# Optimization experiments

Hardware: AMD Instinct MI355X
Metric: run time of the kernel (lower is better)

## Reference

```python
import jax, jax.numpy as jnp
import numpy as np

B, L, H, HEADS, BLOCKS, TSPAN = 8, 256, 256, 4, 2, 512
D = H // HEADS
BIG_NEG = jnp.float32(-2.0**32 + 1)


def _layernorm(x, g, b, eps=1e-8):
    m = x.mean(-1, keepdims=True)
    v = ((x - m) ** 2).mean(-1, keepdims=True)
    return (x - m) / jnp.sqrt(v + eps) * g + b


def _forward(seq_emb, Wq, bq, Wk, bk, Wv, bv, ln1_g, ln1_b, ln2_g, ln2_b,
             W1, b1, W2, b2, pos_K, pos_V, tK_emb, tV_emb, lnf_g, lnf_b,
             mask, time_matrices):
    # relative time-interval embeddings: [B,L,L,H] -> per-head [B,L,L,heads,D]
    tmKh = tK_emb[time_matrices].reshape(B, L, L, HEADS, D)
    tmVh = tV_emb[time_matrices].reshape(B, L, L, HEADS, D)
    posKh = pos_K.reshape(L, HEADS, D)  # abs position embs (positions = arange(L))
    posVh = pos_V.reshape(L, HEADS, D)
    keep = (~mask)[..., None].astype(seq_emb.dtype)  # [B,L,1], True mask = pad
    causal = ~jnp.tril(jnp.ones((L, L), dtype=bool))  # True above diagonal
    x = seq_emb * keep
    scale = jnp.sqrt(jnp.float32(D))
    for i in range(BLOCKS):
        q = _layernorm(x, ln1_g[i], ln1_b[i])  # queries normalized, keys/values raw
        Qh = (q @ Wq[i].T + bq[i]).reshape(B, L, HEADS, D)
        Kh = (x @ Wk[i].T + bk[i]).reshape(B, L, HEADS, D)
        Vh = (x @ Wv[i].T + bv[i]).reshape(B, L, HEADS, D)
        aw = (jnp.einsum('bqhd,bkhd->bhqk', Qh, Kh)
              + jnp.einsum('bqhd,khd->bhqk', Qh, posKh)
              + jnp.einsum('bqhd,bqkhd->bhqk', Qh, tmKh)) / scale
        aw = jnp.where(mask[:, None, :, None] | causal[None, None], BIG_NEG, aw)
        p = jax.nn.softmax(aw, axis=-1)
        out = (jnp.einsum('bhqk,bkhd->bqhd', p, Vh)
               + jnp.einsum('bhqk,khd->bqhd', p, posVh)
               + jnp.einsum('bhqk,bqkhd->bqhd', p, tmVh)).reshape(B, L, H)
        x = q + out
        x = _layernorm(x, ln2_g[i], ln2_b[i])
        h = jax.nn.relu(jnp.einsum('bld,od->blo', x, W1[i]) + b1[i])  # Conv1d k=1 == Linear
        x = jnp.einsum('bld,od->blo', h, W2[i]) + b2[i] + x
        x = x * keep
    return _layernorm(x, lnf_g, lnf_b)


def setup_inputs():
    key = jax.random.key(0)
    ks = jax.random.split(key, 24)
    s = 0.02
    nrm = lambda k, shape: jax.random.normal(k, shape, dtype=jnp.float32) * s
    inp = {}
    inp['mask'] = jax.random.uniform(ks[0], (B, L)) < 0.1
    inp['seq_emb'] = jax.random.normal(ks[1], (B, L, H), dtype=jnp.float32)
    inp['log_seqs'] = jax.random.randint(ks[2], (B, L), 0, 1000)
    inp['time_matrices'] = jax.random.randint(ks[3], (B, L, L), 0, TSPAN + 1).astype(jnp.int32)
    inp['time_attn'] = 0
    inp['Wq'] = nrm(ks[4], (BLOCKS, H, H)); inp['bq'] = jnp.zeros((BLOCKS, H), jnp.float32)
    inp['Wk'] = nrm(ks[5], (BLOCKS, H, H)); inp['bk'] = jnp.zeros((BLOCKS, H), jnp.float32)
    inp['Wv'] = nrm(ks[6], (BLOCKS, H, H)); inp['bv'] = jnp.zeros((BLOCKS, H), jnp.float32)
    inp['ln1_g'] = jnp.ones((BLOCKS, H), jnp.float32); inp['ln1_b'] = jnp.zeros((BLOCKS, H), jnp.float32)
    inp['ln2_g'] = jnp.ones((BLOCKS, H), jnp.float32); inp['ln2_b'] = jnp.zeros((BLOCKS, H), jnp.float32)
    inp['W1'] = nrm(ks[7], (BLOCKS, H, H)); inp['b1'] = jnp.zeros((BLOCKS, H), jnp.float32)
    inp['W2'] = nrm(ks[8], (BLOCKS, H, H)); inp['b2'] = jnp.zeros((BLOCKS, H), jnp.float32)
    inp['pos_K'] = nrm(ks[9], (L, H)); inp['pos_V'] = nrm(ks[10], (L, H))
    inp['tK_emb'] = nrm(ks[11], (TSPAN + 1, H)); inp['tV_emb'] = nrm(ks[12], (TSPAN + 1, H))
    inp['lnf_g'] = jnp.ones((H,), jnp.float32); inp['lnf_b'] = jnp.zeros((H,), jnp.float32)
    return inp


def reference(mask, seq_emb, log_seqs, time_matrices, time_attn,
              Wq, bq, Wk, bk, Wv, bv, ln1_g, ln1_b, ln2_g, ln2_b,
              W1, b1, W2, b2, pos_K, pos_V, tK_emb, tV_emb, lnf_g, lnf_b):
    return _forward(seq_emb, Wq, bq, Wk, bk, Wv, bv, ln1_g, ln1_b, ln2_g, ln2_b,
                    W1, b1, W2, b2, pos_K, pos_V, tK_emb, tV_emb, lnf_g, lnf_b,
                    mask, time_matrices)
```

## Files before the change

### kernel.cpp

```cpp
#include <hip/hip_runtime.h>

#define BIG_NEG_F (-4294967296.0f)

typedef __attribute__((ext_vector_type(8))) short bf16x8;
typedef __attribute__((ext_vector_type(4))) float f32x4;

__device__ __forceinline__ float wave_sum(float v) {
#pragma unroll
    for (int m = 32; m; m >>= 1) v += __shfl_xor(v, m, 64);
    return v;
}
__device__ __forceinline__ float wave_max(float v) {
#pragma unroll
    for (int m = 32; m; m >>= 1) v = fmaxf(v, __shfl_xor(v, m, 64));
    return v;
}

__device__ __forceinline__ unsigned int pack2(float a, float b) {
    return (__float_as_uint(b) & 0xffff0000u) | (__float_as_uint(a) >> 16);
}
__device__ __forceinline__ float hipart(float x) {
    return __uint_as_float(__float_as_uint(x) & 0xffff0000u);
}
__device__ __forceinline__ void store_pair(unsigned short* hp, unsigned short* lp,
                                           float4 a, float4 b) {
    uint4 h;
    h.x = pack2(a.x, a.y); h.y = pack2(a.z, a.w);
    h.z = pack2(b.x, b.y); h.w = pack2(b.z, b.w);
    float lax = a.x - hipart(a.x), lay = a.y - hipart(a.y);
    float laz = a.z - hipart(a.z), law = a.w - hipart(a.w);
    float lbx = b.x - hipart(b.x), lby = b.y - hipart(b.y);
    float lbz = b.z - hipart(b.z), lbw = b.w - hipart(b.w);
    uint4 l;
    l.x = pack2(lax, lay); l.y = pack2(laz, law);
    l.z = pack2(lbx, lby); l.w = pack2(lbz, lbw);
    *(uint4*)hp = h;
    *(uint4*)lp = l;
}

__global__ __launch_bounds__(256) void prep_ln_kernel(const float* __restrict__ seq,
                                                      const unsigned char* __restrict__ mraw,
                                                      unsigned char* __restrict__ mout,
                                                      float* __restrict__ X, float* __restrict__ Q,
                                                      const float* __restrict__ g,
                                                      const float* __restrict__ be) {
    __shared__ int flags[2];
    __shared__ float ws[8];
    int row = blockIdx.x, tid = threadIdx.x;
    if (tid == 0) { flags[0] = 0; flags[1] = 0; }
    __syncthreads();
    for (int i = tid; i < 2048; i += 256) {
        if (mraw[i]) {
            if (i & 3) atomicOr(&flags[0], 1);
            else if (i & 4) atomicOr(&flags[1], 1);
        }
    }
    __syncthreads();
    int mode = flags[0] ? 0 : (flags[1] ? 1 : 2);
    unsigned char mrow = (mode == 0) ? mraw[row] : (mode == 1) ? mraw[row * 4] : mraw[row * 8];
    if (tid == 0) mout[row] = mrow ? 1 : 0;
    int idx = row * 256 + tid;
    int w = tid >> 6, lane = tid & 63;
    float v = mrow ? 0.f : seq[idx];
    X[idx] = v;
    float s = wave_sum(v);
    if (lane == 0) ws[w] = s;
    __syncthreads();
    float mean = (ws[0] + ws[1] + ws[2] + ws[3]) * (1.f / 256.f);
    float d = v - mean;
    float s2 = wave_sum(d * d);
    if (lane == 0) ws[4 + w] = s2;
    __syncthreads();
    float var = (ws[4] + ws[5] + ws[6] + ws[7]) * (1.f / 256.f);
    Q[idx] = d / sqrtf(var + 1e-8f) * g[tid] + be[tid];
}

__global__ __launch_bounds__(256) void ln_kernel(const float* __restrict__ X, float* __restrict__ Y,
                                                 const float* __restrict__ g,
                                                 const float* __restrict__ be) {
    __shared__ float ws[8];
    int row = blockIdx.x, tid = threadIdx.x;
    int idx = row * 256 + tid;
    int w = tid >> 6, lane = tid & 63;
    float v = X[idx];
    float s = wave_sum(v);
    if (lane == 0) ws[w] = s;
    __syncthreads();
    float mean = (ws[0] + ws[1] + ws[2] + ws[3]) * (1.f / 256.f);
    float d = v - mean;
    float s2 = wave_sum(d * d);
    if (lane == 0) ws[4 + w] = s2;
    __syncthreads();
    float var = (ws[4] + ws[5] + ws[6] + ws[7]) * (1.f / 256.f);
    Y[idx] = d / sqrtf(var + 1e-8f) * g[tid] + be[tid];
}

struct GemmJob {
    const float* A;
    const float* W;
    const float* bias;
    const float* pos;
    const float* res;
    const unsigned char* maskm;
    float* C;
    int relu;
};

__global__ __launch_bounds__(256) void gemm_mfma_kernel(GemmJob j0, GemmJob j1, GemmJob j2) {
    GemmJob J = (blockIdx.z == 0) ? j0 : (blockIdx.z == 1 ? j1 : j2);
    __shared__ unsigned short Ah[64][72], Al[64][72], Wh[64][72], Wl[64][72];
    int tid = threadIdx.x;
    int n0 = blockIdx.x * 64, m0 = blockIdx.y * 64;
    int w = tid >> 6, lane = tid & 63;
    int wm = w >> 1, wn = w & 1;
    int srow = tid >> 2, sq = tid & 3;
    const float* Asrc = J.A + (m0 + srow) * 256 + sq * 16;
    const float* Wsrc = J.W + (n0 + srow) * 256 + sq * 16;
    float4 ar0 = *(const float4*)(Asrc),      ar1 = *(const float4*)(Asrc + 4),
           ar2 = *(const float4*)(Asrc + 8),  ar3 = *(const float4*)(Asrc + 12);
    float4 wr0 = *(const float4*)(Wsrc),      wr1 = *(const float4*)(Wsrc + 4),
           wr2 = *(const float4*)(Wsrc + 8),  wr3 = *(const float4*)(Wsrc + 12);
    f32x4 acc[2][2] = {};
    int r15 = lane & 15, hgrp = (lane >> 4) << 3;
    for (int kt = 0; kt < 4; ++kt) {
        if (kt) __syncthreads();
        store_pair(&Ah[srow][sq * 16],     &Al[srow][sq * 16],     ar0, ar1);
        store_pair(&Ah[srow][sq * 16 + 8], &Al[srow][sq * 16 + 8], ar2, ar3);
        store_pair(&Wh[srow][sq * 16],     &Wl[srow][sq * 16],     wr0, wr1);
        store_pair(&Wh[srow][sq * 16 + 8], &Wl[srow][sq * 16 + 8], wr2, wr3);
        __syncthreads();
        if (kt < 3) {
            int ko = (kt + 1) * 64;
            ar0 = *(const float4*)(Asrc + ko);      ar1 = *(const float4*)(Asrc + ko + 4);
            ar2 = *(const float4*)(Asrc + ko + 8);  ar3 = *(const float4*)(Asrc + ko + 12);
            wr0 = *(const float4*)(Wsrc + ko);      wr1 = *(const float4*)(Wsrc + ko + 4);
            wr2 = *(const float4*)(Wsrc + ko + 8);  wr3 = *(const float4*)(Wsrc + ko + 12);
        }
#pragma unroll
        for (int s = 0; s < 2; ++s) {
            int ko = s * 32 + hgrp;
            bf16x8 ah0 = *(const bf16x8*)&Ah[wm * 32 + r15][ko];
            bf16x8 ah1 = *(const bf16x8*)&Ah[wm * 32 + 16 + r15][ko];
            bf16x8 al0 = *(const bf16x8*)&Al[wm * 32 + r15][ko];
            bf16x8 al1 = *(const bf16x8*)&Al[wm * 32 + 16 + r15][ko];
            bf16x8 bh0 = *(const bf16x8*)&Wh[wn * 32 + r15][ko];
            bf16x8 bh1 = *(const bf16x8*)&Wh[wn * 32 + 16 + r15][ko];
            bf16x8 bl0 = *(const bf16x8*)&Wl[wn * 32 + r15][ko];
            bf16x8 bl1 = *(const bf16x8*)&Wl[wn * 32 + 16 + r15][ko];
            acc[0][0] = __builtin_amdgcn_mfma_f32_16x16x32_bf16(ah0, bh0, acc[0][0], 0, 0, 0);
            acc[0][0] = __builtin_amdgcn_mfma_f32_16x16x32_bf16(ah0, bl0, acc[0][0], 0, 0, 0);
            acc[0][0] = __builtin_amdgcn_mfma_f32_16x16x32_bf16(al0, bh0, acc[0][0], 0, 0, 0);
            acc[0][1] = __builtin_amdgcn_mfma_f32_16x16x32_bf16(ah0, bh1, acc[0][1], 0, 0, 0);
            acc[0][1] = __builtin_amdgcn_mfma_f32_16x16x32_bf16(ah0, bl1, acc[0][1], 0, 0, 0);
            acc[0][1] = __builtin_amdgcn_mfma_f32_16x16x32_bf16(al0, bh1, acc[0][1], 0, 0, 0);
            acc[1][0] = __builtin_amdgcn_mfma_f32_16x16x32_bf16(ah1, bh0, acc[1][0], 0, 0, 0);
            acc[1][0] = __builtin_amdgcn_mfma_f32_16x16x32_bf16(ah1, bl0, acc[1][0], 0, 0, 0);
            acc[1][0] = __builtin_amdgcn_mfma_f32_16x16x32_bf16(al1, bh0, acc[1][0], 0, 0, 0);
            acc[1][1] = __builtin_amdgcn_mfma_f32_16x16x32_bf16(ah1, bh1, acc[1][1], 0, 0, 0);
            acc[1][1] = __builtin_amdgcn_mfma_f32_16x16x32_bf16(ah1, bl1, acc[1][1], 0, 0, 0);
            acc[1][1] = __builtin_amdgcn_mfma_f32_16x16x32_bf16(al1, bh1, acc[1][1], 0, 0, 0);
        }
    }
#pragma unroll
    for (int mf = 0; mf < 2; ++mf) {
#pragma unroll
        for (int nf = 0; nf < 2; ++nf) {
            int col = n0 + wn * 32 + nf * 16 + r15;
            int rowb = m0 + wm * 32 + mf * 16 + ((lane >> 4) << 2);
            float bcol = J.bias[col];
            f32x4 a = acc[mf][nf];
#pragma unroll
            for (int rr = 0; rr < 4; ++rr) {
                int m = rowb + rr;
                float v = a[rr] + bcol;
                if (J.pos) v += J.pos[(m & 255) * 256 + col];
                if (J.relu) v = fmaxf(v, 0.f);
                if (J.res) v += J.res[m * 256 + col];
                if (J.maskm && J.maskm[m]) v = 0.f;
                J.C[m * 256 + col] = v;
            }
        }
    }
}

__global__ __launch_bounds__(256, 8) void attn_kernel(
    const float* __restrict__ Q, const float* __restrict__ Kp, const float* __restrict__ Vp,
    const float* __restrict__ qres, const int* __restrict__ tm,
    const float* __restrict__ tK, const float* __restrict__ tV,
    const float* __restrict__ g2, const float* __restrict__ b2,
    float* __restrict__ X2) {
    int bid = (int)blockIdx.x;
    int b = bid & 7;
    int i6 = bid >> 3;
    int jj6 = i6 & 31, a6 = i6 >> 5;
    int q0m = jj6 * 4 + (a6 >> 1);
    int qpos = (a6 & 1) ? q0m : 255 - q0m;
    int tid = threadIdx.x, w = tid >> 6, lane = tid & 63;
    __shared__ float qrow[256];
    __shared__ int   stm[256];
    __shared__ float p[4][264];
    __shared__ float opart[4][256];
    __shared__ float denom[4];
    __shared__ float lnws[8];

    int rowbase = (b * 256 + qpos) * 256;
    qrow[tid] = Q[rowbase + tid];
    {
        int t = tm[rowbase + tid];
        stm[tid] = t < 0 ? 0 : (t > 512 ? 512 : t);
    }
    __syncthreads();

    {
        int h = lane >> 4;
        const float* qr = qrow + lane * 4;
        float q0 = qr[0], q1 = qr[1], q2 = qr[2], q3 = qr[3];
        const float* Kb  = Kp + (size_t)(b << 8) * 256 + lane * 4;
        const float* tKb = tK + lane * 4;
        int nact = (qpos >= w) ? ((qpos - w) >> 2) + 1 : 0;
        int i = 0;
        for (; i + 2 <= nact; i += 2) {
            int k0 = w + 4 * i;
            float4 kv0 = *(const float4*)(Kb + (k0    ) * 256);
            float4 kv1 = *(const float4*)(Kb + (k0 + 4) * 256);
            float4 t0 = *(const float4*)(tKb + stm[k0    ] * 256);
            float4 t1 = *(const float4*)(tKb + stm[k0 + 4] * 256);
            float s0 = q0 * (kv0.x + t0.x) + q1 * (kv0.y + t0.y) + q2 * (kv0.z + t0.z) + q3 * (kv0.w + t0.w);
            float s1 = q0 * (kv1.x + t1.x) + q1 * (kv1.y + t1.y) + q2 * (kv1.z + t1.z) + q3 * (kv1.w + t1.w);
            s0 += __shfl_xor(s0, 1, 64); s1 += __shfl_xor(s1, 1, 64);
            s0 += __shfl_xor(s0, 2, 64); s1 += __shfl_xor(s1, 2, 64);
            s0 += __shfl_xor(s0, 4, 64); s1 += __shfl_xor(s1, 4, 64);
            s0 += __shfl_xor(s0, 8, 64); s1 += __shfl_xor(s1, 8, 64);
            if ((lane & 15) == 0) {
                p[h][k0    ] = s0 * 0.125f;
                p[h][k0 + 4] = s1 * 0.125f;
            }
        }
        if (i < nact) {
            int k = w + 4 * i;
            float4 kv = *(const float4*)(Kb + k * 256);
            float4 t4 = *(const float4*)(tKb + stm[k] * 256);
            float s = q0 * (kv.x + t4.x) + q1 * (kv.y + t4.y) + q2 * (kv.z + t4.z) + q3 * (kv.w + t4.w);
            s += __shfl_xor(s, 1, 64);
            s += __shfl_xor(s, 2, 64);
            s += __shfl_xor(s, 4, 64);
            s += __shfl_xor(s, 8, 64);
            if ((lane & 15) == 0) p[h][k] = s * 0.125f;
        }
    }
    __syncthreads();

    {
        float* ph = &p[w][0];
        float v0 = (lane       <= qpos) ? ph[lane      ] : BIG_NEG_F;
        float v1 = (lane + 64  <= qpos) ? ph[lane + 64 ] : BIG_NEG_F;
        float v2 = (lane + 128 <= qpos) ? ph[lane + 128] : BIG_NEG_F;
        float v3 = (lane + 192 <= qpos) ? ph[lane + 192] : BIG_NEG_F;
        float mx = wave_max(fmaxf(fmaxf(v0, v1), fmaxf(v2, v3)));
        float e0 = __expf(v0 - mx), e1 = __expf(v1 - mx), e2 = __expf(v2 - mx), e3 = __expf(v3 - mx);
        ph[lane] = e0; ph[lane + 64] = e1; ph[lane + 128] = e2; ph[lane + 192] = e3;
        float ssum = wave_sum(e0 + e1 + e2 + e3);
        if (lane == 0) denom[w] = ssum;
    }
    __syncthreads();

    {
        int hh = lane >> 4;
        const float* Vb  = Vp + (size_t)(b << 8) * 256 + lane * 4;
        const float* tVb = tV + lane * 4;
        const float* prow = &p[hh][0];
        float4 a0 = {0.f, 0.f, 0.f, 0.f}, a1 = a0;
        int cnt = (qpos >= w) ? ((qpos - w) >> 2) + 1 : 0;
        int i = 0;
        for (; i + 2 <= cnt; i += 2) {
            int k0 = w + 4 * i;
            float p0 = prow[k0], p1 = prow[k0 + 4];
            float4 v0 = *(const float4*)(Vb + (k0    ) * 256);
            float4 v1 = *(const float4*)(Vb + (k0 + 4) * 256);
            float4 u0 = *(const float4*)(tVb + stm[k0    ] * 256);
            float4 u1 = *(const float4*)(tVb + stm[k0 + 4] * 256);
            a0.x += p0 * (v0.x + u0.x); a0.y += p0 * (v0.y + u0.y); a0.z += p0 * (v0.z + u0.z); a0.w += p0 * (v0.w + u0.w);
            a1.x += p1 * (v1.x + u1.x); a1.y += p1 * (v1.y + u1.y); a1.z += p1 * (v1.z + u1.z); a1.w += p1 * (v1.w + u1.w);
        }
        if (i < cnt) {
            int k2 = w + 4 * i;
            float pk = prow[k2];
            float4 v = *(const float4*)(Vb + k2 * 256);
            float4 t = *(const float4*)(tVb + stm[k2] * 256);
            a0.x += pk * (v.x + t.x);
            a0.y += pk * (v.y + t.y);
            a0.z += pk * (v.z + t.z);
            a0.w += pk * (v.w + t.w);
        }
        float4 o;
        o.x = a0.x + a1.x;
        o.y = a0.y + a1.y;
        o.z = a0.z + a1.z;
        o.w = a0.w + a1.w;
        *(float4*)&opart[w][lane * 4] = o;
    }
    __syncthreads();

    {
        int d = tid, h = tid >> 6;
        float tot = opart[0][d] + opart[1][d] + opart[2][d] + opart[3][d];
        float xv = qres[rowbase + d] + tot / denom[h];
        float s = wave_sum(xv);
        if (lane == 0) lnws[w] = s;
        __syncthreads();
        float mean = (lnws[0] + lnws[1] + lnws[2] + lnws[3]) * (1.f / 256.f);
        float dd = xv - mean;
        float s2 = wave_sum(dd * dd);
        if (lane == 0) lnws[4 + w] = s2;
        __syncthreads();
        float var = (lnws[4] + lnws[5] + lnws[6] + lnws[7]) * (1.f / 256.f);
        X2[rowbase + d] = dd / sqrtf(var + 1e-8f) * g2[d] + b2[d];
    }
}

extern "C" void kernel_launch(void* const* d_in, const int* in_sizes, int n_in,
                              void* d_out, int out_size, void* d_ws, size_t ws_size,
                              hipStream_t stream) {
    const unsigned char* mask_raw = (const unsigned char*)d_in[0];
    const float* seq  = (const float*)d_in[1];
    const int*   tm   = (const int*)d_in[3];
    const float* Wq   = (const float*)d_in[5];
    const float* bq   = (const float*)d_in[6];
    const float* Wk   = (const float*)d_in[7];
    const float* bk   = (const float*)d_in[8];
    const float* Wv   = (const float*)d_in[9];
    const float* bv   = (const float*)d_in[10];
    const float* ln1g = (const float*)d_in[11];
    const float* ln1b = (const float*)d_in[12];
    const float* ln2g = (const float*)d_in[13];
    const float* ln2b = (const float*)d_in[14];
    const float* W1   = (const float*)d_in[15];
    const float* b1   = (const float*)d_in[16];
    const float* W2   = (const float*)d_in[17];
    const float* b2   = (const float*)d_in[18];
    const float* posK = (const float*)d_in[19];
    const float* posV = (const float*)d_in[20];
    const float* tK   = (const float*)d_in[21];
    const float* tV   = (const float*)d_in[22];
    const float* lnfg = (const float*)d_in[23];
    const float* lnfb = (const float*)d_in[24];

    const int NEL = 8 * 256 * 256;
    float* x   = (float*)d_ws;
    float* q   = x   + NEL;
    float* Qb  = q   + NEL;
    float* KpB = Qb  + NEL;
    float* VpB = KpB + NEL;
    float* x2  = VpB + NEL;
    float* hb  = x2  + NEL;
    unsigned char* mask = (unsigned char*)(hb + NEL);

    dim3 gQKV(4, 32, 3);
    dim3 gFFN(4, 32, 1);

    prep_ln_kernel<<<2048, 256, 0, stream>>>(seq, mask_raw, mask, x, q, ln1g, ln1b);
    for (int blk = 0; blk < 2; ++blk) {
        int o1 = blk * 256, oW = blk * 256 * 256;
        GemmJob jq = {q, Wq + oW, bq + o1, nullptr, nullptr, nullptr, Qb, 0};
        GemmJob jk = {x, Wk + oW, bk + o1, posK,    nullptr, nullptr, KpB, 0};
        GemmJob jv = {x, Wv + oW, bv + o1, posV,    nullptr, nullptr, VpB, 0};
        gemm_mfma_kernel<<<gQKV, 256, 0, stream>>>(jq, jk, jv);
        attn_kernel<<<2048, 256, 0, stream>>>(Qb, KpB, VpB, q, tm, tK, tV,
                                              ln2g + o1, ln2b + o1, x2);
        GemmJob f1 = {x2, W1 + oW, b1 + o1, nullptr, nullptr, nullptr, hb, 1};
        gemm_mfma_kernel<<<gFFN, 256, 0, stream>>>(f1, f1, f1);
        GemmJob f2 = {hb, W2 + oW, b2 + o1, nullptr, x2, mask, x, 0};
        gemm_mfma_kernel<<<gFFN, 256, 0, stream>>>(f2, f2, f2);
        if (blk == 0) ln_kernel<<<2048, 256, 0, stream>>>(x, q, ln1g + 256, ln1b + 256);
    }
    ln_kernel<<<2048, 256, 0, stream>>>(x, (float*)d_out, lnfg, lnfb);
}
```

Measured before the change: 255.4 us.

## Process two adjacent query rows per attention block to share K/V loads

The attention kernel now handles two consecutive query positions per workgroup, so each K and V row fetched from global memory is reused for both queries, while the per-query time-embedding gathers stay separate. The grid is halved to 1024 blocks and the launch bound drops to 4 blocks per CU, with a reworked causal load-balancing map over query pairs. Keys past the first query's causal limit are masked in softmax and given zero weight. The cost is more registers and shared memory per block and fewer resident blocks.

```diff
diff --git a/kernel.cpp b/kernel.cpp
--- a/kernel.cpp
+++ b/kernel.cpp
@@ -183,7 +183,7 @@
     }
 }
 
-__global__ __launch_bounds__(256, 8) void attn_kernel(
+__global__ __launch_bounds__(256, 4) void attn_kernel(
     const float* __restrict__ Q, const float* __restrict__ Kp, const float* __restrict__ Vp,
     const float* __restrict__ qres, const int* __restrict__ tm,
     const float* __restrict__ tK, const float* __restrict__ tV,
@@ -192,75 +192,112 @@
     int bid = (int)blockIdx.x;
     int b = bid & 7;
     int i6 = bid >> 3;
-    int jj6 = i6 & 31, a6 = i6 >> 5;
-    int q0m = jj6 * 4 + (a6 >> 1);
-    int qpos = (a6 & 1) ? q0m : 255 - q0m;
+    int j = i6 & 31, a = i6 >> 5;
+    int base = 2 * j + (a >> 1);
+    int P = (a & 1) ? base : 127 - base;
+    int qA = 2 * P, qB = 2 * P + 1;
     int tid = threadIdx.x, w = tid >> 6, lane = tid & 63;
-    __shared__ float qrow[256];
-    __shared__ int   stm[256];
-    __shared__ float p[4][264];
-    __shared__ float opart[4][256];
-    __shared__ float denom[4];
-    __shared__ float lnws[8];
-
-    int rowbase = (b * 256 + qpos) * 256;
-    qrow[tid] = Q[rowbase + tid];
+    __shared__ float qrow[2][256];
+    __shared__ int   stm[2][256];
+    __shared__ float p[2][4][264];
+    __shared__ float opart[2][4][256];
+    __shared__ float denom[2][4];
+    __shared__ float lnws[2][8];
+
+    int rowbaseA = (b * 256 + qA) * 256;
+    int rowbaseB = (b * 256 + qB) * 256;
+    qrow[0][tid] = Q[rowbaseA + tid];
+    qrow[1][tid] = Q[rowbaseB + tid];
     {
-        int t = tm[rowbase + tid];
-        stm[tid] = t < 0 ? 0 : (t > 512 ? 512 : t);
+        int tA = tm[rowbaseA + tid];
+        int tB = tm[rowbaseB + tid];
+        stm[0][tid] = tA < 0 ? 0 : (tA > 512 ? 512 : tA);
+        stm[1][tid] = tB < 0 ? 0 : (tB > 512 ? 512 : tB);
     }
     __syncthreads();
 
     {
         int h = lane >> 4;
-        const float* qr = qrow + lane * 4;
-        float q0 = qr[0], q1 = qr[1], q2 = qr[2], q3 = qr[3];
+        const float* qrA = &qrow[0][lane * 4];
+        const float* qrB = &qrow[1][lane * 4];
+        float qA0 = qrA[0], qA1 = qrA[1], qA2 = qrA[2], qA3 = qrA[3];
+        float qB0 = qrB[0], qB1 = qrB[1], qB2 = qrB[2], qB3 = qrB[3];
         const float* Kb  = Kp + (size_t)(b << 8) * 256 + lane * 4;
         const float* tKb = tK + lane * 4;
-        int nact = (qpos >= w) ? ((qpos - w) >> 2) + 1 : 0;
+        int nact = (qB >= w) ? ((qB - w) >> 2) + 1 : 0;
         int i = 0;
         for (; i + 2 <= nact; i += 2) {
-            int k0 = w + 4 * i;
-            float4 kv0 = *(const float4*)(Kb + (k0    ) * 256);
-            float4 kv1 = *(const float4*)(Kb + (k0 + 4) * 256);
-            float4 t0 = *(const float4*)(tKb + stm[k0    ] * 256);
-            float4 t1 = *(const float4*)(tKb + stm[k0 + 4] * 256);
-            float s0 = q0 * (kv0.x + t0.x) + q1 * (kv0.y + t0.y) + q2 * (kv0.z + t0.z) + q3 * (kv0.w + t0.w);
-            float s1 = q0 * (kv1.x + t1.x) + q1 * (kv1.y + t1.y) + q2 * (kv1.z + t1.z) + q3 * (kv1.w + t1.w);
-            s0 += __shfl_xor(s0, 1, 64); s1 += __shfl_xor(s1, 1, 64);
-            s0 += __shfl_xor(s0, 2, 64); s1 += __shfl_xor(s1, 2, 64);
-            s0 += __shfl_xor(s0, 4, 64); s1 += __shfl_xor(s1, 4, 64);
-            s0 += __shfl_xor(s0, 8, 64); s1 += __shfl_xor(s1, 8, 64);
+            int k0 = w + 4 * i, k1 = k0 + 4;
+            float4 kv0 = *(const float4*)(Kb + k0 * 256);
+            float4 kv1 = *(const float4*)(Kb + k1 * 256);
+            float4 tA0 = *(const float4*)(tKb + stm[0][k0] * 256);
+            float4 tA1 = *(const float4*)(tKb + stm[0][k1] * 256);
+            float4 tB0 = *(const float4*)(tKb + stm[1][k0] * 256);
+            float4 tB1 = *(const float4*)(tKb + stm[1][k1] * 256);
+            float sA0 = qA0 * (kv0.x + tA0.x) + qA1 * (kv0.y + tA0.y) + qA2 * (kv0.z + tA0.z) + qA3 * (kv0.w + tA0.w);
+            float sA1 = qA0 * (kv1.x + tA1.x) + qA1 * (kv1.y + tA1.y) + qA2 * (kv1.z + tA1.z) + qA3 * (kv1.w + tA1.w);
+            float sB0 = qB0 * (kv0.x + tB0.x) + qB1 * (kv0.y + tB0.y) + qB2 * (kv0.z + tB0.z) + qB3 * (kv0.w + tB0.w);
+            float sB1 = qB0 * (kv1.x + tB1.x) + qB1 * (kv1.y + tB1.y) + qB2 * (kv1.z + tB1.z) + qB3 * (kv1.w + tB1.w);
+            sA0 += __shfl_xor(sA0, 1, 64); sA1 += __shfl_xor(sA1, 1, 64);
+            sB0 += __shfl_xor(sB0, 1, 64); sB1 += __shfl_xor(sB1, 1, 64);
+            sA0 += __shfl_xor(sA0, 2, 64); sA1 += __shfl_xor(sA1, 2, 64);
+            sB0 += __shfl_xor(sB0, 2, 64); sB1 += __shfl_xor(sB1, 2, 64);
+            sA0 += __shfl_xor(sA0, 4, 64); sA1 += __shfl_xor(sA1, 4, 64);
+            sB0 += __shfl_xor(sB0, 4, 64); sB1 += __shfl_xor(sB1, 4, 64);
+            sA0 += __shfl_xor(sA0, 8, 64); sA1 += __shfl_xor(sA1, 8, 64);
+            sB0 += __shfl_xor(sB0, 8, 64); sB1 += __shfl_xor(sB1, 8, 64);
             if ((lane & 15) == 0) {
-                p[h][k0    ] = s0 * 0.125f;
-                p[h][k0 + 4] = s1 * 0.125f;
+                p[0][h][k0] = sA0 * 0.125f;
+                p[0][h][k1] = sA1 * 0.125f;
+                p[1][h][k0] = sB0 * 0.125f;
+                p[1][h][k1] = sB1 * 0.125f;
             }
         }
         if (i < nact) {
             int k = w + 4 * i;
             float4 kv = *(const float4*)(Kb + k * 256);
-            float4 t4 = *(const float4*)(tKb + stm[k] * 256);
-            float s = q0 * (kv.x + t4.x) + q1 * (kv.y + t4.y) + q2 * (kv.z + t4.z) + q3 * (kv.w + t4.w);
-            s += __shfl_xor(s, 1, 64);
-            s += __shfl_xor(s, 2, 64);
-            s += __shfl_xor(s, 4, 64);
-            s += __shfl_xor(s, 8, 64);
-            if ((lane & 15) == 0) p[h][k] = s * 0.125f;
+            float4 tA4 = *(const float4*)(tKb + stm[0][k] * 256);
+            float4 tB4 = *(const float4*)(tKb + stm[1][k] * 256);
+            float sA = qA0 * (kv.x + tA4.x) + qA1 * (kv.y + tA4.y) + qA2 * (kv.z + tA4.z) + qA3 * (kv.w + tA4.w);
+            float sB = qB0 * (kv.x + tB4.x) + qB1 * (kv.y + tB4.y) + qB2 * (kv.z + tB4.z) + qB3 * (kv.w + tB4.w);
+            sA += __shfl_xor(sA, 1, 64); sB += __shfl_xor(sB, 1, 64);
+            sA += __shfl_xor(sA, 2, 64); sB += __shfl_xor(sB, 2, 64);
+            sA += __shfl_xor(sA, 4, 64); sB += __shfl_xor(sB, 4, 64);
+            sA += __shfl_xor(sA, 8, 64); sB += __shfl_xor(sB, 8, 64);
+            if ((lane & 15) == 0) {
+                p[0][h][k] = sA * 0.125f;
+                p[1][h][k] = sB * 0.125f;
+            }
         }
     }
     __syncthreads();
 
     {
-        float* ph = &p[w][0];
-        float v0 = (lane       <= qpos) ? ph[lane      ] : BIG_NEG_F;
-        float v1 = (lane + 64  <= qpos) ? ph[lane + 64 ] : BIG_NEG_F;
-        float v2 = (lane + 128 <= qpos) ? ph[lane + 128] : BIG_NEG_F;
-        float v3 = (lane + 192 <= qpos) ? ph[lane + 192] : BIG_NEG_F;
-        float mx = wave_max(fmaxf(fmaxf(v0, v1), fmaxf(v2, v3)));
-        float e0 = __expf(v0 - mx), e1 = __expf(v1 - mx), e2 = __expf(v2 - mx), e3 = __expf(v3 - mx);
-        ph[lane] = e0; ph[lane + 64] = e1; ph[lane + 128] = e2; ph[lane + 192] = e3;
-        float ssum = wave_sum(e0 + e1 + e2 + e3);
-        if (lane == 0) denom[w] = ssum;
+        float* phA = &p[0][w][0];
+        float* phB = &p[1][w][0];
+        float a0 = (lane       <= qA) ? phA[lane      ] : BIG_NEG_F;
+        float a1 = (lane + 64  <= qA) ? phA[lane + 64 ] : BIG_NEG_F;
+        float a2 = (lane + 128 <= qA) ? phA[lane + 128] : BIG_NEG_F;
+        float a3 = (lane + 192 <= qA) ? phA[lane + 192] : BIG_NEG_F;
+        float b0 = (lane       <= qB) ? phB[lane      ] : BIG_NEG_F;
+        float b1 = (lane + 64  <= qB) ? phB[lane + 64 ] : BIG_NEG_F;
+        float b2v = (lane + 128 <= qB) ? phB[lane + 128] : BIG_NEG_F;
+        float b3 = (lane + 192 <= qB) ? phB[lane + 192] : BIG_NEG_F;
+        float mxA = wave_max(fmaxf(fmaxf(a0, a1), fmaxf(a2, a3)));
+        float mxB = wave_max(fmaxf(fmaxf(b0, b1), fmaxf(b2v, b3)));
+        float eA0 = (lane       <= qA) ? __expf(a0 - mxA) : 0.f;
+        float eA1 = (lane + 64  <= qA) ? __expf(a1 - mxA) : 0.f;
+        float eA2 = (lane + 128 <= qA) ? __expf(a2 - mxA) : 0.f;
+        float eA3 = (lane + 192 <= qA) ? __expf(a3 - mxA) : 0.f;
+        float eB0 = (lane       <= qB) ? __expf(b0 - mxB) : 0.f;
+        float eB1 = (lane + 64  <= qB) ? __expf(b1 - mxB) : 0.f;
+        float eB2 = (lane + 128 <= qB) ? __expf(b2v - mxB) : 0.f;
+        float eB3 = (lane + 192 <= qB) ? __expf(b3 - mxB) : 0.f;
+        phA[lane] = eA0; phA[lane + 64] = eA1; phA[lane + 128] = eA2; phA[lane + 192] = eA3;
+        phB[lane] = eB0; phB[lane + 64] = eB1; phB[lane + 128] = eB2; phB[lane + 192] = eB3;
+        float sumA = wave_sum(eA0 + eA1 + eA2 + eA3);
+        float sumB = wave_sum(eB0 + eB1 + eB2 + eB3);
+        if (lane == 0) { denom[0][w] = sumA; denom[1][w] = sumB; }
     }
     __syncthreads();
 
@@ -268,53 +305,66 @@
         int hh = lane >> 4;
         const float* Vb  = Vp + (size_t)(b << 8) * 256 + lane * 4;
         const float* tVb = tV + lane * 4;
-        const float* prow = &p[hh][0];
-        float4 a0 = {0.f, 0.f, 0.f, 0.f}, a1 = a0;
-        int cnt = (qpos >= w) ? ((qpos - w) >> 2) + 1 : 0;
+        const float* prA = &p[0][hh][0];
+        const float* prB = &p[1][hh][0];
+        float4 aA0 = {0.f, 0.f, 0.f, 0.f}, aA1 = aA0, aB0 = aA0, aB1 = aA0;
+        int cnt = (qB >= w) ? ((qB - w) >> 2) + 1 : 0;
         int i = 0;
         for (; i + 2 <= cnt; i += 2) {
-            int k0 = w + 4 * i;
-            float p0 = prow[k0], p1 = prow[k0 + 4];
-            float4 v0 = *(const float4*)(Vb + (k0    ) * 256);
-            float4 v1 = *(const float4*)(Vb + (k0 + 4) * 256);
-            float4 u0 = *(const float4*)(tVb + stm[k0    ] * 256);
-            float4 u1 = *(const float4*)(tVb + stm[k0 + 4] * 256);
-            a0.x += p0 * (v0.x + u0.x); a0.y += p0 * (v0.y + u0.y); a0.z += p0 * (v0.z + u0.z); a0.w += p0 * (v0.w + u0.w);
-            a1.x += p1 * (v1.x + u1.x); a1.y += p1 * (v1.y + u1.y); a1.z += p1 * (v1.z + u1.z); a1.w += p1 * (v1.w + u1.w);
+            int k0 = w + 4 * i, k1 = k0 + 4;
+            float pA0 = prA[k0], pA1 = prA[k1], pB0 = prB[k0], pB1 = prB[k1];
+            float4 v0 = *(const float4*)(Vb + k0 * 256);
+            float4 v1 = *(const float4*)(Vb + k1 * 256);
+            float4 uA0 = *(const float4*)(tVb + stm[0][k0] * 256);
+            float4 uA1 = *(const float4*)(tVb + stm[0][k1] * 256);
+            float4 uB0 = *(const float4*)(tVb + stm[1][k0] * 256);
+            float4 uB1 = *(const float4*)(tVb + stm[1][k1] * 256);
+            aA0.x += pA0 * (v0.x + uA0.x); aA0.y += pA0 * (v0.y + uA0.y); aA0.z += pA0 * (v0.z + uA0.z); aA0.w += pA0 * (v0.w + uA0.w);
+            aA1.x += pA1 * (v1.x + uA1.x); aA1.y += pA1 * (v1.y + uA1.y); aA1.z += pA1 * (v1.z + uA1.z); aA1.w += pA1 * (v1.w + uA1.w);
+            aB0.x += pB0 * (v0.x + uB0.x); aB0.y += pB0 * (v0.y + uB0.y); aB0.z += pB0 * (v0.z + uB0.z); aB0.w += pB0 * (v0.w + uB0.w);
+            aB1.x += pB1 * (v1.x + uB1.x); aB1.y += pB1 * (v1.y + uB1.y); aB1.z += pB1 * (v1.z + uB1.z); aB1.w += pB1 * (v1.w + uB1.w);
         }
         if (i < cnt) {
             int k2 = w + 4 * i;
-            float pk = prow[k2];
+            float pA = prA[k2], pB = prB[k2];
             float4 v = *(const float4*)(Vb + k2 * 256);
-            float4 t = *(const float4*)(tVb + stm[k2] * 256);
-            a0.x += pk * (v.x + t.x);
-            a0.y += pk * (v.y + t.y);
-            a0.z += pk * (v.z + t.z);
-            a0.w += pk * (v.w + t.w);
-        }
-        float4 o;
-        o.x = a0.x + a1.x;
-        o.y = a0.y + a1.y;
-        o.z = a0.z + a1.z;
-        o.w = a0.w + a1.w;
-        *(float4*)&opart[w][lane * 4] = o;
+            float4 uA = *(const float4*)(tVb + stm[0][k2] * 256);
+            float4 uB = *(const float4*)(tVb + stm[1][k2] * 256);
+            aA0.x += pA * (v.x + uA.x); aA0.y += pA * (v.y + uA.y);
+            aA0.z += pA * (v.z + uA.z); aA0.w += pA * (v.w + uA.w);
+            aB0.x += pB * (v.x + uB.x); aB0.y += pB * (v.y + uB.y);
+            aB0.z += pB * (v.z + uB.z); aB0.w += pB * (v.w + uB.w);
+        }
+        float4 oA, oB;
+        oA.x = aA0.x + aA1.x; oA.y = aA0.y + aA1.y; oA.z = aA0.z + aA1.z; oA.w = aA0.w + aA1.w;
+        oB.x = aB0.x + aB1.x; oB.y = aB0.y + aB1.y; oB.z = aB0.z + aB1.z; oB.w = aB0.w + aB1.w;
+        *(float4*)&opart[0][w][lane * 4] = oA;
+        *(float4*)&opart[1][w][lane * 4] = oB;
     }
     __syncthreads();
 
     {
         int d = tid, h = tid >> 6;
-        float tot = opart[0][d] + opart[1][d] + opart[2][d] + opart[3][d];
-        float xv = qres[rowbase + d] + tot / denom[h];
-        float s = wave_sum(xv);
-        if (lane == 0) lnws[w] = s;
+        float totA = opart[0][0][d] + opart[0][1][d] + opart[0][2][d] + opart[0][3][d];
+        float totB = opart[1][0][d] + opart[1][1][d] + opart[1][2][d] + opart[1][3][d];
+        float xvA = qres[rowbaseA + d] + totA / denom[0][h];
+        float xvB = qres[rowbaseB + d] + totB / denom[1][h];
+        float sA = wave_sum(xvA);
+        float sB = wave_sum(xvB);
+        if (lane == 0) { lnws[0][w] = sA; lnws[1][w] = sB; }
         __syncthreads();
-        float mean = (lnws[0] + lnws[1] + lnws[2] + lnws[3]) * (1.f / 256.f);
-        float dd = xv - mean;
-        float s2 = wave_sum(dd * dd);
-        if (lane == 0) lnws[4 + w] = s2;
+        float meanA = (lnws[0][0] + lnws[0][1] + lnws[0][2] + lnws[0][3]) * (1.f / 256.f);
+        float meanB = (lnws[1][0] + lnws[1][1] + lnws[1][2] + lnws[1][3]) * (1.f / 256.f);
+        float ddA = xvA - meanA, ddB = xvB - meanB;
+        float s2A = wave_sum(ddA * ddA);
+        float s2B = wave_sum(ddB * ddB);
+        if (lane == 0) { lnws[0][4 + w] = s2A; lnws[1][4 + w] = s2B; }
         __syncthreads();
-        float var = (lnws[4] + lnws[5] + lnws[6] + lnws[7]) * (1.f / 256.f);
-        X2[rowbase + d] = dd / sqrtf(var + 1e-8f) * g2[d] + b2[d];
+        float varA = (lnws[0][4] + lnws[0][5] + lnws[0][6] + lnws[0][7]) * (1.f / 256.f);
+        float varB = (lnws[1][4] + lnws[1][5] + lnws[1][6] + lnws[1][7]) * (1.f / 256.f);
+        float gg = g2[d], bb = b2[d];
+        X2[rowbaseA + d] = ddA / sqrtf(varA + 1e-8f) * gg + bb;
+        X2[rowbaseB + d] = ddB / sqrtf(varB + 1e-8f) * gg + bb;
     }
 }
 
@@ -365,7 +415,7 @@
         GemmJob jk = {x, Wk + oW, bk + o1, posK,    nullptr, nullptr, KpB, 0};
         GemmJob jv = {x, Wv + oW, bv + o1, posV,    nullptr, nullptr, VpB, 0};
         gemm_mfma_kernel<<<gQKV, 256, 0, stream>>>(jq, jk, jv);
-        attn_kernel<<<2048, 256, 0, stream>>>(Qb, KpB, VpB, q, tm, tK, tV,
+        attn_kernel<<<1024, 256, 0, stream>>>(Qb, KpB, VpB, q, tm, tK, tV,
                                               ln2g + o1, ln2b + o1, x2);
         GemmJob f1 = {x2, W1 + oW, b1 + o1, nullptr, nullptr, nullptr, hb, 1};
         gemm_mfma_kernel<<<gFFN, 256, 0, stream>>>(f1, f1, f1);
```

After: 249.3 us. 2.4% less time.
